# Kernel optimization log

Hardware: AMD Instinct MI355X
Metric: run time of the kernel (lower is better)

The kernel has to match this reference:

```python
import jax, jax.numpy as jnp
import numpy as np

COEF_MEMORY = 0.2

def setup_inputs() -> dict:
    key = jax.random.key(0)
    k1, k2, k3, k4 = jax.random.split(key, 4)
    B, T, HW, C, Cv, M = 2, 8, 4096, 64, 3, 1024
    k = jax.random.normal(k1, (B, T, HW, C), dtype=jnp.float32)
    v = jax.random.normal(k2, (B, T, HW, Cv), dtype=jnp.float32)
    m_k = jax.random.normal(k3, (B, T - 1, M, C), dtype=jnp.float32)
    m_v = jax.random.normal(k4, (B, T - 1, M, Cv), dtype=jnp.float32)
    return {"k": k, "v": v, "m_k": m_k, "m_v": m_v}

def reference(k, v, m_k, m_v):
    # k: [B,T,HW,C] frame keys; v: [B,T,HW,Cv] frame values (quarter-res images)
    # m_k: [B,T-1,M,C] memory keys at step i; m_v: [B,T-1,M,Cv] memory values
    c = COEF_MEMORY
    k_i = k[:, :-1]  # ref keys  [B,T-1,HW,C]
    k_j = k[:, 1:]   # tar keys  [B,T-1,HW,C]
    v_i = v[:, :-1]  # ref vals  [B,T-1,HW,Cv]
    # frame-to-frame affinity: softmax over ref positions (last axis)
    sim_k = jax.nn.softmax(jnp.einsum('btqc,btkc->btqk', k_j, k_i), axis=-1)
    # memory-to-frame affinity: softmax over memory slots
    sim_m = jax.nn.softmax(jnp.einsum('btqc,btmc->btqm', k_j, m_k), axis=-1)
    rec_k = jnp.einsum('btqk,btkd->btqd', sim_k, v_i)   # [B,T-1,HW,Cv]
    rec_m = jnp.einsum('btqm,btmd->btqd', sim_m, m_v)   # [B,T-1,HW,Cv]
    return (1.0 - c) * rec_k + c * rec_m
```

## Files before the change

kernel.cpp:

```cpp
#include <hip/hip_runtime.h>

typedef __attribute__((ext_vector_type(2))) __fp16 h2;
typedef __attribute__((ext_vector_type(4))) __fp16 h4;
typedef __attribute__((ext_vector_type(8))) __fp16 h8;
typedef __attribute__((ext_vector_type(4))) float f32x4;

#define LOG2E 1.44269504088896340736f

#define WS_K    0ull
#define WS_MK   7340032ull
#define WS_VT   9175040ull
#define WS_MVT  9633792ull
#define WS_NEED 9748480ull

__device__ __forceinline__ h2 pkrtz(float a, float b) {
    return __builtin_bit_cast(h2, __builtin_amdgcn_cvt_pkrtz(a, b));
}

__global__ __launch_bounds__(256) void kast_pre_kernel(
    const float* __restrict__ K, const float* __restrict__ V,
    const float* __restrict__ MK, const float* __restrict__ MV,
    char* __restrict__ ws)
{
    const int id = blockIdx.x * 256 + threadIdx.x;
    if (id < 573440) {
        const bool ismk = id >= 458752;
        const int lid = ismk ? id - 458752 : id;
        const int c = lid & 7;
        const int r = (lid >> 3) & 63;
        int kt, s;
        if (ismk) { kt = (lid >> 9) & 15; s = lid >> 13; }
        else      { kt = (lid >> 9) & 63; s = lid >> 15; }
        const int b = s / 7, t = s - b * 7;
        const float* src = ismk
            ? MK + (((size_t)(b * 7 + t) * 1024 + kt * 64 + r) * 64 + c * 8)
            : K  + (((size_t)(b * 8 + t) * 4096 + kt * 64 + r) * 64 + c * 8);
        const f32x4 xa = *(const f32x4*)src;
        const f32x4 xb = *(const f32x4*)(src + 4);
        const h2 q0 = pkrtz(xa[0], xa[1]), q1 = pkrtz(xa[2], xa[3]);
        const h2 q2 = pkrtz(xb[0], xb[1]), q3 = pkrtz(xb[2], xb[3]);
        const h8 out = {q0[0], q0[1], q1[0], q1[1], q2[0], q2[1], q3[0], q3[1]};
        __fp16* dst = (__fp16*)(ws + (ismk ? WS_MK : WS_K))
                    + (size_t)(ismk ? (s * 16 + kt) : (s * 64 + kt)) * 4096
                    + r * 64 + ((c ^ (r & 7)) * 8);
        *(h8*)dst = out;
    } else {
        const int vid = id - 573440;
        const bool ismv = vid >= 57344;
        const int lid = ismv ? vid - 57344 : vid;
        const int c = lid & 15;
        const int d = (lid >> 4) & 3;
        int kt, s;
        if (ismv) { kt = (lid >> 6) & 15; s = lid >> 10; }
        else      { kt = (lid >> 6) & 63; s = lid >> 12; }
        const int b = s / 7, t = s - b * 7;
        const float* src = ismv
            ? MV + (((size_t)(b * 7 + t) * 1024 + kt * 64 + c * 4) * 3)
            : V  + (((size_t)(b * 8 + t) * 4096 + kt * 64 + c * 4) * 3);
        float f0, f1, f2, f3;
        if (d == 3) { f0 = f1 = f2 = f3 = 1.0f; }
        else { f0 = src[d]; f1 = src[3 + d]; f2 = src[6 + d]; f3 = src[9 + d]; }
        const h2 pa = pkrtz(f0, f1), pb = pkrtz(f2, f3);
        const h4 out4 = {pa[0], pa[1], pb[0], pb[1]};
        __fp16* dst = (__fp16*)(ws + (ismv ? WS_MVT : WS_VT))
                    + (size_t)(ismv ? (s * 16 + kt) : (s * 64 + kt)) * 256
                    + d * 64 + (4 * ((c >> 2) ^ d) + (c & 3)) * 4;
        *(h4*)dst = out4;
    }
}

__global__ __launch_bounds__(256, 4) void kast_attn_kernel(
    const float* __restrict__ K,
    const char* __restrict__ ws,
    float* __restrict__ OUT)
{
    __shared__ float mrg[4][32][5];

    const int id = blockIdx.x;
    const int sw = (id & 7) * 224 + (id >> 3);
    const int bt = sw >> 7;
    const int qblk = sw & 127;
    const int b = bt / 7, t = bt - b * 7;

    const int tid = threadIdx.x;
    const int lane = tid & 63;
    const int w = tid >> 6;
    const int col = lane & 15;
    const int g = lane >> 4;
    const int cs = col & 7;
    const int d3 = col & 3;

    const int a00 = col * 128 + ((g ^ cs) * 16);
    const int a10 = col * 128 + (((4 + g) ^ cs) * 16);
    const int ov0 = (4 * (0 ^ d3) + g) * 8;
    const int ov1 = (4 * (1 ^ d3) + g) * 8;
    const int ov2 = (4 * (2 ^ d3) + g) * 8;
    const int ov3 = (4 * (3 ^ d3) + g) * 8;

    h8 aq00, aq01, aq10, aq11;
    {
        const float* qp0 = K + (((size_t)b * 8 + (t + 1)) * 4096
                          + (size_t)(qblk * 32 + col)) * 64;
        const float* qp1 = qp0 + 16 * 64;
#pragma unroll
        for (int mt = 0; mt < 2; ++mt) {
            const float* qp = mt ? qp1 : qp0;
#pragma unroll
            for (int ch = 0; ch < 2; ++ch) {
                const int cc = ch * 32 + g * 8;
                const f32x4 xa = *(const f32x4*)&qp[cc];
                const f32x4 xb = *(const f32x4*)&qp[cc + 4];
                const h2 p0 = pkrtz(xa[0] * LOG2E, xa[1] * LOG2E);
                const h2 p1 = pkrtz(xa[2] * LOG2E, xa[3] * LOG2E);
                const h2 p2 = pkrtz(xb[0] * LOG2E, xb[1] * LOG2E);
                const h2 p3 = pkrtz(xb[2] * LOG2E, xb[3] * LOG2E);
                const h8 f = {p0[0], p0[1], p1[0], p1[1], p2[0], p2[1], p3[0], p3[1]};
                if (mt == 0 && ch == 0) aq00 = f;
                else if (mt == 0)       aq01 = f;
                else if (ch == 0)       aq10 = f;
                else                    aq11 = f;
            }
        }
    }

    float oa0 = 0.f, oa1 = 0.f, oa2 = 0.f;

#pragma unroll
    for (int phase = 0; phase < 2; ++phase) {
        const int n = phase ? 8 : 32;
        const float wgt = phase ? 0.2f : 0.8f;
        const char* kbase = phase
            ? ws + WS_MK  + (size_t)bt * 131072 + (size_t)w * 32768
            : ws + WS_K   + (size_t)bt * 524288 + (size_t)w * 131072;
        const char* vbase = (phase
            ? ws + WS_MVT + (size_t)bt * 8192  + (size_t)w * 2048
            : ws + WS_VT  + (size_t)bt * 32768 + (size_t)w * 8192) + d3 * 128;

        float mrun0 = -1e30f, mrun1 = -1e30f;
        f32x4 O0 = (f32x4){0.f,0.f,0.f,0.f}, O1 = (f32x4){0.f,0.f,0.f,0.f};

        h8 kA00, kA01, kA10, kA11; h4 vA0, vA1;
        {
            const char* tb = kbase;
            kA00 = *(const h8*)(tb + a00);
            kA01 = *(const h8*)(tb + a00 + 2048);
            kA10 = *(const h8*)(tb + a10);
            kA11 = *(const h8*)(tb + a10 + 2048);
            vA0 = *(const h4*)(vbase + ov0);
            vA1 = *(const h4*)(vbase + ov1);
        }

#define COMPUTE(kf00, kf01, kf10, kf11, v0, v1)                                   \
        {                                                                         \
            f32x4 c00 = (f32x4){0.f,0.f,0.f,0.f}, c01 = c00, c10 = c00, c11 = c00;\
            __builtin_amdgcn_s_setprio(1);                                        \
            c00 = __builtin_amdgcn_mfma_f32_16x16x32_f16(kf00, aq00, c00, 0,0,0); \
            c01 = __builtin_amdgcn_mfma_f32_16x16x32_f16(kf01, aq00, c01, 0,0,0); \
            c10 = __builtin_amdgcn_mfma_f32_16x16x32_f16(kf00, aq10, c10, 0,0,0); \
            c11 = __builtin_amdgcn_mfma_f32_16x16x32_f16(kf01, aq10, c11, 0,0,0); \
            c00 = __builtin_amdgcn_mfma_f32_16x16x32_f16(kf10, aq01, c00, 0,0,0); \
            c01 = __builtin_amdgcn_mfma_f32_16x16x32_f16(kf11, aq01, c01, 0,0,0); \
            c10 = __builtin_amdgcn_mfma_f32_16x16x32_f16(kf10, aq11, c10, 0,0,0); \
            c11 = __builtin_amdgcn_mfma_f32_16x16x32_f16(kf11, aq11, c11, 0,0,0); \
            __builtin_amdgcn_s_setprio(0);                                        \
            float tm0 = fmaxf(fmaxf(fmaxf(c00[0], c00[1]), fmaxf(c00[2], c00[3])),\
                              fmaxf(fmaxf(c01[0], c01[1]), fmaxf(c01[2], c01[3])));\
            float tm1 = fmaxf(fmaxf(fmaxf(c10[0], c10[1]), fmaxf(c10[2], c10[3])),\
                              fmaxf(fmaxf(c11[0], c11[1]), fmaxf(c11[2], c11[3])));\
            float s0 = __shfl_xor(tm0, 16), s1 = __shfl_xor(tm1, 16);             \
            tm0 = fmaxf(tm0, s0); tm1 = fmaxf(tm1, s1);                           \
            s0 = __shfl_xor(tm0, 32); s1 = __shfl_xor(tm1, 32);                   \
            tm0 = fmaxf(tm0, s0); tm1 = fmaxf(tm1, s1);                           \
            const float m0 = fmaxf(mrun0, tm0), m1 = fmaxf(mrun1, tm1);           \
            const float r0 = __builtin_amdgcn_exp2f(mrun0 - m0);                  \
            const float r1 = __builtin_amdgcn_exp2f(mrun1 - m1);                  \
            O0 *= r0; O1 *= r1; mrun0 = m0; mrun1 = m1;                           \
            {                                                                     \
                const float e0 = __builtin_amdgcn_exp2f(c00[0] - mrun0);          \
                const float e1 = __builtin_amdgcn_exp2f(c00[1] - mrun0);          \
                const float e2 = __builtin_amdgcn_exp2f(c00[2] - mrun0);          \
                const float e3 = __builtin_amdgcn_exp2f(c00[3] - mrun0);          \
                const h2 pa = pkrtz(e0, e1), pb = pkrtz(e2, e3);                  \
                const h4 pf = (h4){pa[0], pa[1], pb[0], pb[1]};                   \
                O0 = __builtin_amdgcn_mfma_f32_16x16x16f16(v0, pf, O0, 0, 0, 0);  \
            }                                                                     \
            {                                                                     \
                const float e0 = __builtin_amdgcn_exp2f(c01[0] - mrun0);          \
                const float e1 = __builtin_amdgcn_exp2f(c01[1] - mrun0);          \
                const float e2 = __builtin_amdgcn_exp2f(c01[2] - mrun0);          \
                const float e3 = __builtin_amdgcn_exp2f(c01[3] - mrun0);          \
                const h2 pa = pkrtz(e0, e1), pb = pkrtz(e2, e3);                  \
                const h4 pf = (h4){pa[0], pa[1], pb[0], pb[1]};                   \
                O0 = __builtin_amdgcn_mfma_f32_16x16x16f16(v1, pf, O0, 0, 0, 0);  \
            }                                                                     \
            {                                                                     \
                const float e0 = __builtin_amdgcn_exp2f(c10[0] - mrun1);          \
                const float e1 = __builtin_amdgcn_exp2f(c10[1] - mrun1);          \
                const float e2 = __builtin_amdgcn_exp2f(c10[2] - mrun1);          \
                const float e3 = __builtin_amdgcn_exp2f(c10[3] - mrun1);          \
                const h2 pa = pkrtz(e0, e1), pb = pkrtz(e2, e3);                  \
                const h4 pf = (h4){pa[0], pa[1], pb[0], pb[1]};                   \
                O1 = __builtin_amdgcn_mfma_f32_16x16x16f16(v0, pf, O1, 0, 0, 0);  \
            }                                                                     \
            {                                                                     \
                const float e0 = __builtin_amdgcn_exp2f(c11[0] - mrun1);          \
                const float e1 = __builtin_amdgcn_exp2f(c11[1] - mrun1);          \
                const float e2 = __builtin_amdgcn_exp2f(c11[2] - mrun1);          \
                const float e3 = __builtin_amdgcn_exp2f(c11[3] - mrun1);          \
                const h2 pa = pkrtz(e0, e1), pb = pkrtz(e2, e3);                  \
                const h4 pf = (h4){pa[0], pa[1], pb[0], pb[1]};                   \
                O1 = __builtin_amdgcn_mfma_f32_16x16x16f16(v1, pf, O1, 0, 0, 0);  \
            }                                                                     \
        }

        for (int kt = 0; kt < n; kt += 2) {
            h8 kB00, kB01, kB10, kB11; h4 vB0, vB1;
            {
                const char* tb = kbase + (size_t)(kt + 1) * 4096;
                kB00 = *(const h8*)(tb + a00);
                kB01 = *(const h8*)(tb + a00 + 2048);
                kB10 = *(const h8*)(tb + a10);
                kB11 = *(const h8*)(tb + a10 + 2048);
                const char* vt = vbase + (size_t)(kt >> 1) * 512;
                vB0 = *(const h4*)(vt + ov2);
                vB1 = *(const h4*)(vt + ov3);
            }
            COMPUTE(kA00, kA01, kA10, kA11, vA0, vA1);
            if (kt + 2 < n) {
                const char* tb = kbase + (size_t)(kt + 2) * 4096;
                kA00 = *(const h8*)(tb + a00);
                kA01 = *(const h8*)(tb + a00 + 2048);
                kA10 = *(const h8*)(tb + a10);
                kA11 = *(const h8*)(tb + a10 + 2048);
                const char* vt = vbase + (size_t)((kt + 2) >> 1) * 512;
                vA0 = *(const h4*)(vt + ov0);
                vA1 = *(const h4*)(vt + ov1);
            }
            COMPUTE(kB00, kB01, kB10, kB11, vB0, vB1);
        }
#undef COMPUTE

        if (g == 0) {
            float* m5a = &mrg[w][col][0];
            m5a[0] = mrun0;
            m5a[1] = O0[0]; m5a[2] = O0[1]; m5a[3] = O0[2]; m5a[4] = O0[3];
            float* m5b = &mrg[w][16 + col][0];
            m5b[0] = mrun1;
            m5b[1] = O1[0]; m5b[2] = O1[1]; m5b[3] = O1[2]; m5b[4] = O1[3];
        }
        __syncthreads();
        if (tid < 32) {
            float m = -1e30f;
#pragma unroll
            for (int q4 = 0; q4 < 4; ++q4) m = fmaxf(m, mrg[q4][tid][0]);
            float l = 0.f, r0 = 0.f, r1 = 0.f, r2 = 0.f;
#pragma unroll
            for (int q4 = 0; q4 < 4; ++q4) {
                const float* m5 = &mrg[q4][tid][0];
                const float e = __builtin_amdgcn_exp2f(m5[0] - m);
                r0 += m5[1] * e; r1 += m5[2] * e; r2 += m5[3] * e;
                l  += m5[4] * e;
            }
            const float inv = wgt / l;
            oa0 += r0 * inv; oa1 += r1 * inv; oa2 += r2 * inv;
        }
        __syncthreads();
    }

    if (tid < 32) {
        const int q = qblk * 32 + tid;
        float* op = OUT + (((size_t)b * 7 + t) * 4096 + (size_t)q) * 3;
        op[0] = oa0; op[1] = oa1; op[2] = oa2;
    }
}

__global__ __launch_bounds__(256) void kast_attn_fb(
    const float* __restrict__ K, const float* __restrict__ V,
    const float* __restrict__ MK, const float* __restrict__ MV,
    float* __restrict__ OUT)
{
    __shared__ alignas(16) __fp16 sK[2][64][64];
    __shared__ alignas(16) __fp16 sVT[2][4][68];

    const int id = blockIdx.x;
    const int sw = (id & 7) * 112 + (id >> 3);
    const int bt = sw >> 6;
    const int qblk = sw & 63;
    const int b = bt / 7, t = bt % 7;

    const int tid = threadIdx.x;
    const int lane = tid & 63;
    const int w = tid >> 6;
    const int col = lane & 15;
    const int g = lane >> 4;

    const int r = tid >> 2;
    const int c0 = (tid & 3) * 16;
    const int rs = (r & 7) << 3;
    const unsigned vr = (unsigned)tid / 3u;
    const unsigned vd = (unsigned)tid - vr * 3u;

    if (tid < 128) sVT[tid >> 6][3][tid & 63] = (__fp16)1.0f;

    const float* Qbase = K + (((size_t)b * 8 + (t + 1)) * 4096) * 64;
    h8 aq[2];
    {
        const int qrow = qblk * 64 + w * 16 + col;
        const float* qp = Qbase + (size_t)qrow * 64;
#pragma unroll
        for (int ch = 0; ch < 2; ++ch) {
            const int cc = ch * 32 + g * 8;
            const f32x4 xa = *(const f32x4*)&qp[cc];
            const f32x4 xb = *(const f32x4*)&qp[cc + 4];
            const h2 p0 = pkrtz(xa[0] * LOG2E, xa[1] * LOG2E);
            const h2 p1 = pkrtz(xa[2] * LOG2E, xa[3] * LOG2E);
            const h2 p2 = pkrtz(xb[0] * LOG2E, xb[1] * LOG2E);
            const h2 p3 = pkrtz(xb[2] * LOG2E, xb[3] * LOG2E);
            aq[ch] = (h8){p0[0], p0[1], p1[0], p1[1], p2[0], p2[1], p3[0], p3[1]};
        }
    }

    float outc0 = 0.f, outc1 = 0.f, outc2 = 0.f;

    for (int phase = 0; phase < 2; ++phase) {
        const float* kp; const float* vp; int ntile; float wgt;
        if (phase == 0) {
            kp = K + (((size_t)b * 8 + t) * 4096) * 64;
            vp = V + (((size_t)b * 8 + t) * 4096) * 3;
            ntile = 64; wgt = 0.8f;
        } else {
            kp = MK + (((size_t)b * 7 + t) * 1024) * 64;
            vp = MV + (((size_t)b * 7 + t) * 1024) * 3;
            ntile = 16; wgt = 0.2f;
        }
        {
            const float* src = kp + ((size_t)r) * 64 + c0;
            const f32x4* s4 = (const f32x4*)src;
            const f32x4 ra = s4[0], rb = s4[1], rc = s4[2], rd = s4[3];
            const h2 q0 = pkrtz(ra[0], ra[1]), q1 = pkrtz(ra[2], ra[3]);
            const h2 q2 = pkrtz(rb[0], rb[1]), q3 = pkrtz(rb[2], rb[3]);
            const h2 q4 = pkrtz(rc[0], rc[1]), q5 = pkrtz(rc[2], rc[3]);
            const h2 q6 = pkrtz(rd[0], rd[1]), q7 = pkrtz(rd[2], rd[3]);
            *(h8*)&sK[0][r][c0 ^ rs] = (h8){q0[0], q0[1], q1[0], q1[1], q2[0], q2[1], q3[0], q3[1]};
            *(h8*)&sK[0][r][(c0 + 8) ^ rs] = (h8){q4[0], q4[1], q5[0], q5[1], q6[0], q6[1], q7[0], q7[1]};
            if (tid < 192) sVT[0][vd][vr] = (__fp16)vp[tid];
        }
        __syncthreads();

        float mrun = -1e30f;
        f32x4 O = (f32x4){0.f, 0.f, 0.f, 0.f};

        for (int kt = 0; kt < ntile; ++kt) {
            const int cur = kt & 1;
            const bool have = (kt + 1) < ntile;
            f32x4 ra, rb, rc, rd; float rv = 0.f;
            if (have) {
                const float* src = kp + ((size_t)(kt + 1) * 64 + r) * 64 + c0;
                const f32x4* s4 = (const f32x4*)src;
                ra = s4[0]; rb = s4[1]; rc = s4[2]; rd = s4[3];
                if (tid < 192) rv = vp[(size_t)(kt + 1) * 192 + tid];
            }
            f32x4 acc[4];
#pragma unroll
            for (int nt = 0; nt < 4; ++nt) acc[nt] = (f32x4){0.f, 0.f, 0.f, 0.f};
#pragma unroll
            for (int ch = 0; ch < 2; ++ch) {
                h8 bh[4];
#pragma unroll
                for (int nt = 0; nt < 4; ++nt) {
                    const int rr = nt * 16 + col;
                    const int cc = (ch * 32 + g * 8) ^ ((rr & 7) << 3);
                    bh[nt] = *(const h8*)&sK[cur][rr][cc];
                }
#pragma unroll
                for (int nt = 0; nt < 4; ++nt)
                    acc[nt] = __builtin_amdgcn_mfma_f32_16x16x32_f16(bh[nt], aq[ch], acc[nt], 0, 0, 0);
            }
            {
                float tm = acc[0][0];
#pragma unroll
                for (int nt = 0; nt < 4; ++nt)
#pragma unroll
                    for (int j = 0; j < 4; ++j) tm = fmaxf(tm, acc[nt][j]);
                tm = fmaxf(tm, __shfl_xor(tm, 16));
                tm = fmaxf(tm, __shfl_xor(tm, 32));
                if (!__all(tm <= mrun)) {
                    const float mnew = fmaxf(mrun, tm);
                    const float sc = __builtin_amdgcn_exp2f(mrun - mnew);
                    O *= sc;
                    mrun = mnew;
                }
            }
#pragma unroll
            for (int nt = 0; nt < 4; ++nt) {
                const float p0 = __builtin_amdgcn_exp2f(acc[nt][0] - mrun);
                const float p1 = __builtin_amdgcn_exp2f(acc[nt][1] - mrun);
                const float p2 = __builtin_amdgcn_exp2f(acc[nt][2] - mrun);
                const float p3 = __builtin_amdgcn_exp2f(acc[nt][3] - mrun);
                const h2 pa = pkrtz(p0, p1), pb = pkrtz(p2, p3);
                const h4 pf = (h4){pa[0], pa[1], pb[0], pb[1]};
                const h4 vf = *(const h4*)&sVT[cur][col & 3][nt * 16 + 4 * g];
                O = __builtin_amdgcn_mfma_f32_16x16x16f16(vf, pf, O, 0, 0, 0);
            }
            if (have) {
                const int nb = cur ^ 1;
                const h2 q0 = pkrtz(ra[0], ra[1]), q1 = pkrtz(ra[2], ra[3]);
                const h2 q2 = pkrtz(rb[0], rb[1]), q3 = pkrtz(rb[2], rb[3]);
                const h2 q4 = pkrtz(rc[0], rc[1]), q5 = pkrtz(rc[2], rc[3]);
                const h2 q6 = pkrtz(rd[0], rd[1]), q7 = pkrtz(rd[2], rd[3]);
                *(h8*)&sK[nb][r][c0 ^ rs] = (h8){q0[0], q0[1], q1[0], q1[1], q2[0], q2[1], q3[0], q3[1]};
                *(h8*)&sK[nb][r][(c0 + 8) ^ rs] = (h8){q4[0], q4[1], q5[0], q5[1], q6[0], q6[1], q7[0], q7[1]};
                if (tid < 192) sVT[nb][vd][vr] = (__fp16)rv;
            }
            __syncthreads();
        }
        const float inv = wgt / O[3];
        outc0 += O[0] * inv;
        outc1 += O[1] * inv;
        outc2 += O[2] * inv;
    }

    if (g == 0) {
        const int q = qblk * 64 + w * 16 + col;
        float* op = OUT + (((size_t)b * 7 + t) * 4096 + (size_t)q) * 3;
        op[0] = outc0; op[1] = outc1; op[2] = outc2;
    }
}

extern "C" void kernel_launch(void* const* d_in, const int* in_sizes, int n_in,
                              void* d_out, int out_size, void* d_ws, size_t ws_size,
                              hipStream_t stream) {
    const float* K  = (const float*)d_in[0];
    const float* V  = (const float*)d_in[1];
    const float* MK = (const float*)d_in[2];
    const float* MV = (const float*)d_in[3];
    float* OUT = (float*)d_out;
    if (ws_size >= WS_NEED) {
        hipLaunchKernelGGL(kast_pre_kernel, dim3(2520), dim3(256), 0, stream,
                           K, V, MK, MV, (char*)d_ws);
        hipLaunchKernelGGL(kast_attn_kernel, dim3(1792), dim3(256), 0, stream,
                           K, (const char*)d_ws, OUT);
    } else {
        hipLaunchKernelGGL(kast_attn_fb, dim3(896), dim3(256), 0, stream,
                           K, V, MK, MV, OUT);
    }
}
```

Baseline: 98.29 us.

## Software-pipeline QK MFMA of next tile with softmax/PV of current tile

Restructures the inner attention loop so the QK^T MFMAs for tile i+1 are issued before the softmax exponentials and PV MFMAs of tile i. This lets the matrix unit work alongside the exp/max VALU work and the cross-lane shuffles, and hides MFMA latency, instead of running each tile's phases back to back. It costs extra registers for two sets of score accumulators and K fragments, which may lower occupancy or cause spills.

```diff
diff --git a/kernel.cpp b/kernel.cpp
--- a/kernel.cpp
+++ b/kernel.cpp
@@ -139,34 +139,40 @@
         float mrun0 = -1e30f, mrun1 = -1e30f;
         f32x4 O0 = (f32x4){0.f,0.f,0.f,0.f}, O1 = (f32x4){0.f,0.f,0.f,0.f};
 
-        h8 kA00, kA01, kA10, kA11; h4 vA0, vA1;
-        {
-            const char* tb = kbase;
-            kA00 = *(const h8*)(tb + a00);
-            kA01 = *(const h8*)(tb + a00 + 2048);
-            kA10 = *(const h8*)(tb + a10);
-            kA11 = *(const h8*)(tb + a10 + 2048);
-            vA0 = *(const h4*)(vbase + ov0);
-            vA1 = *(const h4*)(vbase + ov1);
-        }
-
-#define COMPUTE(kf00, kf01, kf10, kf11, v0, v1)                                   \
+        h8 f0_00, f0_01, f0_10, f0_11;
+        h8 f1_00, f1_01, f1_10, f1_11;
+        h4 vA0, vA1, vB0, vB1;
+        f32x4 cA00, cA01, cA10, cA11;
+        f32x4 cB00, cB01, cB10, cB11;
+
+#define LOADF0(TKT) { const char* tb = kbase + (size_t)(TKT) * 4096;              \
+            f0_00 = *(const h8*)(tb + a00); f0_01 = *(const h8*)(tb + a00 + 2048);\
+            f0_10 = *(const h8*)(tb + a10); f0_11 = *(const h8*)(tb + a10 + 2048); }
+#define LOADF1(TKT) { const char* tb = kbase + (size_t)(TKT) * 4096;              \
+            f1_00 = *(const h8*)(tb + a00); f1_01 = *(const h8*)(tb + a00 + 2048);\
+            f1_10 = *(const h8*)(tb + a10); f1_11 = *(const h8*)(tb + a10 + 2048); }
+
+#define QK(F00, F01, F10, F11, C00, C01, C10, C11)                                \
         {                                                                         \
-            f32x4 c00 = (f32x4){0.f,0.f,0.f,0.f}, c01 = c00, c10 = c00, c11 = c00;\
+            C00 = (f32x4){0.f,0.f,0.f,0.f}; C01 = C00; C10 = C00; C11 = C00;      \
             __builtin_amdgcn_s_setprio(1);                                        \
-            c00 = __builtin_amdgcn_mfma_f32_16x16x32_f16(kf00, aq00, c00, 0,0,0); \
-            c01 = __builtin_amdgcn_mfma_f32_16x16x32_f16(kf01, aq00, c01, 0,0,0); \
-            c10 = __builtin_amdgcn_mfma_f32_16x16x32_f16(kf00, aq10, c10, 0,0,0); \
-            c11 = __builtin_amdgcn_mfma_f32_16x16x32_f16(kf01, aq10, c11, 0,0,0); \
-            c00 = __builtin_amdgcn_mfma_f32_16x16x32_f16(kf10, aq01, c00, 0,0,0); \
-            c01 = __builtin_amdgcn_mfma_f32_16x16x32_f16(kf11, aq01, c01, 0,0,0); \
-            c10 = __builtin_amdgcn_mfma_f32_16x16x32_f16(kf10, aq11, c10, 0,0,0); \
-            c11 = __builtin_amdgcn_mfma_f32_16x16x32_f16(kf11, aq11, c11, 0,0,0); \
+            C00 = __builtin_amdgcn_mfma_f32_16x16x32_f16(F00, aq00, C00, 0,0,0);  \
+            C01 = __builtin_amdgcn_mfma_f32_16x16x32_f16(F01, aq00, C01, 0,0,0);  \
+            C10 = __builtin_amdgcn_mfma_f32_16x16x32_f16(F00, aq10, C10, 0,0,0);  \
+            C11 = __builtin_amdgcn_mfma_f32_16x16x32_f16(F01, aq10, C11, 0,0,0);  \
+            C00 = __builtin_amdgcn_mfma_f32_16x16x32_f16(F10, aq01, C00, 0,0,0);  \
+            C01 = __builtin_amdgcn_mfma_f32_16x16x32_f16(F11, aq01, C01, 0,0,0);  \
+            C10 = __builtin_amdgcn_mfma_f32_16x16x32_f16(F10, aq11, C10, 0,0,0);  \
+            C11 = __builtin_amdgcn_mfma_f32_16x16x32_f16(F11, aq11, C11, 0,0,0);  \
             __builtin_amdgcn_s_setprio(0);                                        \
-            float tm0 = fmaxf(fmaxf(fmaxf(c00[0], c00[1]), fmaxf(c00[2], c00[3])),\
-                              fmaxf(fmaxf(c01[0], c01[1]), fmaxf(c01[2], c01[3])));\
-            float tm1 = fmaxf(fmaxf(fmaxf(c10[0], c10[1]), fmaxf(c10[2], c10[3])),\
-                              fmaxf(fmaxf(c11[0], c11[1]), fmaxf(c11[2], c11[3])));\
+        }
+
+#define SMPV(C00, C01, C10, C11, V0, V1)                                          \
+        {                                                                         \
+            float tm0 = fmaxf(fmaxf(fmaxf(C00[0], C00[1]), fmaxf(C00[2], C00[3])),\
+                              fmaxf(fmaxf(C01[0], C01[1]), fmaxf(C01[2], C01[3])));\
+            float tm1 = fmaxf(fmaxf(fmaxf(C10[0], C10[1]), fmaxf(C10[2], C10[3])),\
+                              fmaxf(fmaxf(C11[0], C11[1]), fmaxf(C11[2], C11[3])));\
             float s0 = __shfl_xor(tm0, 16), s1 = __shfl_xor(tm1, 16);             \
             tm0 = fmaxf(tm0, s0); tm1 = fmaxf(tm1, s1);                           \
             s0 = __shfl_xor(tm0, 32); s1 = __shfl_xor(tm1, 32);                   \
@@ -176,69 +182,70 @@
             const float r1 = __builtin_amdgcn_exp2f(mrun1 - m1);                  \
             O0 *= r0; O1 *= r1; mrun0 = m0; mrun1 = m1;                           \
             {                                                                     \
-                const float e0 = __builtin_amdgcn_exp2f(c00[0] - mrun0);          \
-                const float e1 = __builtin_amdgcn_exp2f(c00[1] - mrun0);          \
-                const float e2 = __builtin_amdgcn_exp2f(c00[2] - mrun0);          \
-                const float e3 = __builtin_amdgcn_exp2f(c00[3] - mrun0);          \
+                const float e0 = __builtin_amdgcn_exp2f(C00[0] - mrun0);          \
+                const float e1 = __builtin_amdgcn_exp2f(C00[1] - mrun0);          \
+                const float e2 = __builtin_amdgcn_exp2f(C00[2] - mrun0);          \
+                const float e3 = __builtin_amdgcn_exp2f(C00[3] - mrun0);          \
                 const h2 pa = pkrtz(e0, e1), pb = pkrtz(e2, e3);                  \
                 const h4 pf = (h4){pa[0], pa[1], pb[0], pb[1]};                   \
-                O0 = __builtin_amdgcn_mfma_f32_16x16x16f16(v0, pf, O0, 0, 0, 0);  \
+                O0 = __builtin_amdgcn_mfma_f32_16x16x16f16(V0, pf, O0, 0, 0, 0);  \
             }                                                                     \
             {                                                                     \
-                const float e0 = __builtin_amdgcn_exp2f(c01[0] - mrun0);          \
-                const float e1 = __builtin_amdgcn_exp2f(c01[1] - mrun0);          \
-                const float e2 = __builtin_amdgcn_exp2f(c01[2] - mrun0);          \
-                const float e3 = __builtin_amdgcn_exp2f(c01[3] - mrun0);          \
+                const float e0 = __builtin_amdgcn_exp2f(C01[0] - mrun0);          \
+                const float e1 = __builtin_amdgcn_exp2f(C01[1] - mrun0);          \
+                const float e2 = __builtin_amdgcn_exp2f(C01[2] - mrun0);          \
+                const float e3 = __builtin_amdgcn_exp2f(C01[3] - mrun0);          \
                 const h2 pa = pkrtz(e0, e1), pb = pkrtz(e2, e3);                  \
                 const h4 pf = (h4){pa[0], pa[1], pb[0], pb[1]};                   \
-                O0 = __builtin_amdgcn_mfma_f32_16x16x16f16(v1, pf, O0, 0, 0, 0);  \
+                O0 = __builtin_amdgcn_mfma_f32_16x16x16f16(V1, pf, O0, 0, 0, 0);  \
             }                                                                     \
             {                                                                     \
-                const float e0 = __builtin_amdgcn_exp2f(c10[0] - mrun1);          \
-                const float e1 = __builtin_amdgcn_exp2f(c10[1] - mrun1);          \
-                const float e2 = __builtin_amdgcn_exp2f(c10[2] - mrun1);          \
-                const float e3 = __builtin_amdgcn_exp2f(c10[3] - mrun1);          \
+                const float e0 = __builtin_amdgcn_exp2f(C10[0] - mrun1);          \
+                const float e1 = __builtin_amdgcn_exp2f(C10[1] - mrun1);          \
+                const float e2 = __builtin_amdgcn_exp2f(C10[2] - mrun1);          \
+                const float e3 = __builtin_amdgcn_exp2f(C10[3] - mrun1);          \
                 const h2 pa = pkrtz(e0, e1), pb = pkrtz(e2, e3);                  \
                 const h4 pf = (h4){pa[0], pa[1], pb[0], pb[1]};                   \
-                O1 = __builtin_amdgcn_mfma_f32_16x16x16f16(v0, pf, O1, 0, 0, 0);  \
+                O1 = __builtin_amdgcn_mfma_f32_16x16x16f16(V0, pf, O1, 0, 0, 0);  \
             }                                                                     \
             {                                                                     \
-                const float e0 = __builtin_amdgcn_exp2f(c11[0] - mrun1);          \
-                const float e1 = __builtin_amdgcn_exp2f(c11[1] - mrun1);          \
-                const float e2 = __builtin_amdgcn_exp2f(c11[2] - mrun1);          \
-                const float e3 = __builtin_amdgcn_exp2f(c11[3] - mrun1);          \
+                const float e0 = __builtin_amdgcn_exp2f(C11[0] - mrun1);          \
+                const float e1 = __builtin_amdgcn_exp2f(C11[1] - mrun1);          \
+                const float e2 = __builtin_amdgcn_exp2f(C11[2] - mrun1);          \
+                const float e3 = __builtin_amdgcn_exp2f(C11[3] - mrun1);          \
                 const h2 pa = pkrtz(e0, e1), pb = pkrtz(e2, e3);                  \
                 const h4 pf = (h4){pa[0], pa[1], pb[0], pb[1]};                   \
-                O1 = __builtin_amdgcn_mfma_f32_16x16x16f16(v1, pf, O1, 0, 0, 0);  \
+                O1 = __builtin_amdgcn_mfma_f32_16x16x16f16(V1, pf, O1, 0, 0, 0);  \
             }                                                                     \
         }
 
+        LOADF0(0);
+        LOADF1(1);
+        vA0 = *(const h4*)(vbase + ov0); vA1 = *(const h4*)(vbase + ov1);
+        vB0 = *(const h4*)(vbase + ov2); vB1 = *(const h4*)(vbase + ov3);
+        QK(f0_00, f0_01, f0_10, f0_11, cA00, cA01, cA10, cA11);
+
         for (int kt = 0; kt < n; kt += 2) {
-            h8 kB00, kB01, kB10, kB11; h4 vB0, vB1;
-            {
-                const char* tb = kbase + (size_t)(kt + 1) * 4096;
-                kB00 = *(const h8*)(tb + a00);
-                kB01 = *(const h8*)(tb + a00 + 2048);
-                kB10 = *(const h8*)(tb + a10);
-                kB11 = *(const h8*)(tb + a10 + 2048);
-                const char* vt = vbase + (size_t)(kt >> 1) * 512;
-                vB0 = *(const h4*)(vt + ov2);
-                vB1 = *(const h4*)(vt + ov3);
-            }
-            COMPUTE(kA00, kA01, kA10, kA11, vA0, vA1);
-            if (kt + 2 < n) {
-                const char* tb = kbase + (size_t)(kt + 2) * 4096;
-                kA00 = *(const h8*)(tb + a00);
-                kA01 = *(const h8*)(tb + a00 + 2048);
-                kA10 = *(const h8*)(tb + a10);
-                kA11 = *(const h8*)(tb + a10 + 2048);
+            const bool more = (kt + 2) < n;
+            if (more) LOADF0(kt + 2);
+            QK(f1_00, f1_01, f1_10, f1_11, cB00, cB01, cB10, cB11);
+            SMPV(cA00, cA01, cA10, cA11, vA0, vA1);
+            if (more) {
+                LOADF1(kt + 3);
                 const char* vt = vbase + (size_t)((kt + 2) >> 1) * 512;
-                vA0 = *(const h4*)(vt + ov0);
-                vA1 = *(const h4*)(vt + ov1);
-            }
-            COMPUTE(kB00, kB01, kB10, kB11, vB0, vB1);
-        }
-#undef COMPUTE
+                vA0 = *(const h4*)(vt + ov0); vA1 = *(const h4*)(vt + ov1);
+                QK(f0_00, f0_01, f0_10, f0_11, cA00, cA01, cA10, cA11);
+            }
+            SMPV(cB00, cB01, cB10, cB11, vB0, vB1);
+            if (more) {
+                const char* vt = vbase + (size_t)((kt + 2) >> 1) * 512;
+                vB0 = *(const h4*)(vt + ov2); vB1 = *(const h4*)(vt + ov3);
+            }
+        }
+#undef LOADF0
+#undef LOADF1
+#undef QK
+#undef SMPV
 
         if (g == 0) {
             float* m5a = &mrg[w][col][0];
```

Result: slower. 103.4 us (+5.2%).
